# Kernel tuning notes

Measured on AMD Instinct MI355X. Metric: run time of the kernel, lower is better.

## Reference

```python
import jax, jax.numpy as jnp
import numpy as np

N_EXP, N_EMBD = 8, 1024
D_FF = 4 * N_EMBD
TOK = 2048  # tokens per expert


def setup_inputs() -> dict:
    key = jax.random.key(0)
    k_x, k_fc, k_pr, k_fb, k_pb = jax.random.split(key, 5)
    scale = 0.02
    return {
        "x": jax.random.normal(k_x, (N_EXP, TOK, N_EMBD), dtype=jnp.float32),
        "c_fc": jax.random.normal(k_fc, (N_EXP, N_EMBD, D_FF), dtype=jnp.float32) * scale,
        "c_proj": jax.random.normal(k_pr, (N_EXP, D_FF, N_EMBD), dtype=jnp.float32) * scale,
        "fc_bias": jax.random.normal(k_fb, (N_EXP, 1, D_FF), dtype=jnp.float32) * scale,
        "proj_bias": jax.random.normal(k_pb, (N_EXP, 1, N_EMBD), dtype=jnp.float32) * scale,
    }


def reference(x, c_fc, c_proj, fc_bias, proj_bias):
    # grouped GEMM over experts: [e, t, d] @ [e, d, f] -> [e, t, f]
    h = jnp.einsum('etd,edf->etf', x, c_fc) + fc_bias
    h = jax.nn.gelu(h, approximate=False)  # torch nn.GELU default is exact erf
    out = jnp.einsum('etf,efd->etd', h, c_proj) + proj_bias
    # dropout p=0.0 (eval): identity
    return out
```

## Files before the change

### kernel.cpp

```cpp
#include <hip/hip_runtime.h>
#include <cmath>

typedef __bf16 bf16;
typedef __bf16 bf16x8 __attribute__((ext_vector_type(8)));
typedef float floatx4 __attribute__((ext_vector_type(4)));

#define E_ 8
#define M_ 2048
#define D_ 1024
#define F_ 4096

#define PUNROLL _Pragma("unroll")

__device__ __forceinline__ void async16(const void* g, void* l) {
    __builtin_amdgcn_global_load_lds((const __attribute__((address_space(1))) unsigned int*)g,
                                     (__attribute__((address_space(3))) unsigned int*)l, 16, 0, 0);
}

__device__ __forceinline__ float gelu_fast(float u) {
    float s = u * (-1.5957691216f - 0.0713548162726f * u * u);
    return u * __builtin_amdgcn_rcpf(1.0f + __expf(s));
}

__device__ __forceinline__ void tconv_body(const float* __restrict__ in, bf16* __restrict__ out,
                                           int R, int C, int bx, int by, int bz,
                                           float (*t)[65]) {
    size_t eoff = (size_t)bz * R * C;
    in += eoff;
    out += eoff;
    const int c0 = bx * 64, r0 = by * 64;
    const int tid = threadIdx.x;
    const int f4c = tid & 15;
    const int rsub = tid >> 4;
    PUNROLL
    for (int p = 0; p < 4; ++p) {
        int row = rsub + p * 16;
        float4 v = *(const float4*)&in[(size_t)(r0 + row) * C + c0 + f4c * 4];
        t[row][f4c * 4 + 0] = v.x;
        t[row][f4c * 4 + 1] = v.y;
        t[row][f4c * 4 + 2] = v.z;
        t[row][f4c * 4 + 3] = v.w;
    }
    __syncthreads();
    const int rr = (tid & 7) * 8;
    const int cbase = tid >> 3;
    PUNROLL
    for (int p = 0; p < 2; ++p) {
        int c = cbase + p * 32;
        bf16x8 o = {(bf16)t[rr + 0][c], (bf16)t[rr + 1][c], (bf16)t[rr + 2][c],
                    (bf16)t[rr + 3][c], (bf16)t[rr + 4][c], (bf16)t[rr + 5][c],
                    (bf16)t[rr + 6][c], (bf16)t[rr + 7][c]};
        *(bf16x8*)&out[(size_t)(c0 + c) * R + r0 + rr] = o;
    }
}

__device__ __forceinline__ void xconv_body(const float4* __restrict__ x, bf16x8* __restrict__ xb,
                                           int b, int nblk) {
    const int n8 = E_ * M_ * D_ / 8;
    int i = b * 256 + threadIdx.x;
    for (; i < n8; i += nblk * 256) {
        float4 a = x[2 * i], c = x[2 * i + 1];
        bf16x8 r = {(bf16)a.x, (bf16)a.y, (bf16)a.z, (bf16)a.w,
                    (bf16)c.x, (bf16)c.y, (bf16)c.z, (bf16)c.w};
        xb[i] = r;
    }
}

__global__ __launch_bounds__(256) void prep_all(const float4* __restrict__ x,
                                                bf16x8* __restrict__ xb,
                                                const float* __restrict__ c_fc,
                                                bf16* __restrict__ w1T,
                                                const float* __restrict__ c_proj,
                                                bf16* __restrict__ w2T) {
    __shared__ float t[64][65];
    const int b = blockIdx.x;
    if (b < 2048) {
        xconv_body(x, xb, b, 2048);
    } else if (b < 10240) {
        const int idx = b - 2048;
        tconv_body(c_fc, w1T, D_, F_, idx & 63, (idx >> 6) & 15, idx >> 10, t);
    } else {
        const int idx = b - 10240;
        tconv_body(c_proj, w2T, F_, D_, idx & 15, (idx >> 4) & 63, idx >> 10, t);
    }
}

__global__ __launch_bounds__(256) void prep_kernel(const float4* __restrict__ x,
                                                   bf16x8* __restrict__ xb,
                                                   const float* __restrict__ c_fc,
                                                   bf16* __restrict__ w1T) {
    __shared__ float t[64][65];
    const int b = blockIdx.x;
    if (b < 2048) {
        xconv_body(x, xb, b, 2048);
    } else {
        const int idx = b - 2048;
        tconv_body(c_fc, w1T, D_, F_, idx & 63, (idx >> 6) & 15, idx >> 10, t);
    }
}

__global__ __launch_bounds__(256) void tconv2_kernel(const float* __restrict__ in,
                                                     bf16* __restrict__ out) {
    __shared__ float t[64][65];
    const int idx = blockIdx.x;
    tconv_body(in, out, F_, D_, idx & 15, (idx >> 4) & 63, idx >> 10, t);
}

template <bool GELU>
__global__ __launch_bounds__(512, 2) void gemm256(const bf16* __restrict__ A0,
                                                  const bf16* __restrict__ Bt0,
                                                  const float* __restrict__ bias0,
                                                  void* __restrict__ Out,
                                                  int M, int N, int K, int tpb) {
    extern __shared__ __align__(16) char sm[];
    const int nt = K >> 6;
    const int NTm = M >> 8;
    const int NTn = N >> 8;
    const int nwg = gridDim.x;
    const int bid = blockIdx.x;
    const int swz = (bid & 7) * (nwg >> 3) + (bid >> 3);

    const int tid = threadIdx.x;
    const int l = tid & 63;
    const int w = tid >> 6;
    const int wm = w >> 2;
    const int wn = w & 3;

    const size_t Kb = (size_t)K * 2;
    const size_t half128 = 128 * Kb;
    const size_t j64 = 64 * Kb;
    const int srow = (w << 3) + (l >> 3);
    const int kb = ((l & 7) ^ ((l >> 3) & 7)) << 4;
    const int ldsW = w << 10;

    auto stage = [&](int hb, const char* src, int ko) {
        async16(src + ko, sm + hb + ldsW);
        async16(src + j64 + ko, sm + hb + 8192 + ldsW);
    };
    auto prologue = [&](const char* aS, const char* bS) {
        stage(0, aS, 0);
        stage(32768, bS, 0);
        stage(49152, bS + half128, 0);
        stage(16384, aS + half128, 0);
        stage(65536 + 0, aS, 128);
        stage(65536 + 32768, bS, 128);
        stage(65536 + 49152, bS + half128, 128);
    };

    const int kpat0 = (((l >> 4) << 4)) ^ ((l & 7) << 4);
    const int kpat1 = (64 + ((l >> 4) << 4)) ^ ((l & 7) << 4);
    const int aRowOff = (((wm << 6) + (l & 15)) << 7);
    const int bRowOff = (((wn << 5) + (l & 15)) << 7);

    int tile = swz * tpb;
    int tm = tile % NTm, rem = tile / NTm;
    int tn = rem % NTn, e = rem / NTn;
    int row0 = tm << 8, col0 = tn << 8;
    const char* aS = (const char*)A0 + ((size_t)e * M + row0 + srow) * Kb + kb;
    const char* bS = (const char*)Bt0 + ((size_t)e * N + col0 + srow) * Kb + kb;
    prologue(aS, bS);

    for (int j = 0; j < tpb; ++j) {
        asm volatile("s_waitcnt vmcnt(6)" ::: "memory");
        __builtin_amdgcn_s_barrier();

        bf16x8 aa[4][2];
        bf16x8 bb0[2][2], bb1[2][2];
        floatx4 acc00[4][2] = {}, acc01[4][2] = {}, acc10[4][2] = {}, acc11[4][2] = {};

#define READ_A(QM)                                                                          \
    PUNROLL                                                                                 \
    for (int mi = 0; mi < 4; ++mi) {                                                        \
        aa[mi][0] = *(const bf16x8*)(sm + p + (QM)*16384 + aRowOff + mi * 2048 + kpat0);    \
        aa[mi][1] = *(const bf16x8*)(sm + p + (QM)*16384 + aRowOff + mi * 2048 + kpat1);    \
    }
#define READ_B(BB, QN)                                                                      \
    PUNROLL                                                                                 \
    for (int ni = 0; ni < 2; ++ni) {                                                        \
        BB[ni][0] = *(const bf16x8*)(sm + p + 32768 + (QN)*16384 + bRowOff + ni * 2048 + kpat0); \
        BB[ni][1] = *(const bf16x8*)(sm + p + 32768 + (QN)*16384 + bRowOff + ni * 2048 + kpat1); \
    }
#define MQ(ACC, BB)                                                                         \
    PUNROLL                                                                                 \
    for (int mi = 0; mi < 4; ++mi) PUNROLL for (int ni = 0; ni < 2; ++ni) {                 \
        ACC[mi][ni] = __builtin_amdgcn_mfma_f32_16x16x32_bf16(aa[mi][0], BB[ni][0], ACC[mi][ni], 0, 0, 0); \
        ACC[mi][ni] = __builtin_amdgcn_mfma_f32_16x16x32_bf16(aa[mi][1], BB[ni][1], ACC[mi][ni], 0, 0, 0); \
    }

        for (int t = 0; t < nt; ++t) {
            const int p = (t & 1) << 16;
            const int pn = p ^ 65536;
            const int ko1 = (t + 1) << 7;
            const int ko2 = (t + 2) << 7;
            READ_A(0)
            READ_B(bb0, 0)
            if (t + 1 < nt) stage(pn + 16384, aS + half128, ko1);
            __builtin_amdgcn_s_barrier();
            __builtin_amdgcn_s_setprio(1);
            MQ(acc00, bb0)
            __builtin_amdgcn_s_setprio(0);
            __builtin_amdgcn_s_barrier();
            READ_B(bb1, 1)
            if (t + 2 < nt) stage(p + 0, aS, ko2);
            __builtin_amdgcn_s_barrier();
            __builtin_amdgcn_s_setprio(1);
            MQ(acc01, bb1)
            __builtin_amdgcn_s_setprio(0);
            __builtin_amdgcn_s_barrier();
            READ_A(1)
            if (t + 2 < nt) stage(p + 32768, bS, ko2);
            __builtin_amdgcn_s_barrier();
            __builtin_amdgcn_s_setprio(1);
            MQ(acc11, bb1)
            __builtin_amdgcn_s_setprio(0);
            __builtin_amdgcn_s_barrier();
            if (t + 2 < nt) {
                stage(p + 49152, bS + half128, ko2);
                asm volatile("s_waitcnt vmcnt(6)" ::: "memory");
            } else if (t + 1 < nt) {
                asm volatile("s_waitcnt vmcnt(0)" ::: "memory");
            }
            __builtin_amdgcn_s_barrier();
            __builtin_amdgcn_s_setprio(1);
            MQ(acc10, bb0)
            __builtin_amdgcn_s_setprio(0);
            __builtin_amdgcn_s_barrier();
        }

        const int erow0 = row0, ecol0 = col0;
        const float* ebias = bias0 + (size_t)e * N;
        const size_t eout = (size_t)e * M * N;
        if (j + 1 < tpb) {
            tile = swz * tpb + j + 1;
            tm = tile % NTm; rem = tile / NTm;
            tn = rem % NTn; e = rem / NTn;
            row0 = tm << 8; col0 = tn << 8;
            aS = (const char*)A0 + ((size_t)e * M + row0 + srow) * Kb + kb;
            bS = (const char*)Bt0 + ((size_t)e * N + col0 + srow) * Kb + kb;
            prologue(aS, bS);
        }

#define EPI(ACC, QM, QN)                                                                    \
    PUNROLL                                                                                 \
    for (int ni = 0; ni < 2; ++ni) {                                                        \
        const int col = ecol0 + (QN)*128 + (wn << 5) + ni * 16 + (l & 15);                  \
        const float bv = ebias[col];                                                        \
        PUNROLL                                                                             \
        for (int mi = 0; mi < 4; ++mi) {                                                    \
            const int row = erow0 + (QM)*128 + (wm << 6) + mi * 16 + ((l >> 4) << 2);       \
            PUNROLL                                                                         \
            for (int r = 0; r < 4; ++r) {                                                   \
                float v = ACC[mi][ni][r] + bv;                                              \
                if (GELU)                                                                   \
                    ((bf16*)Out)[eout + (size_t)(row + r) * N + col] = (bf16)gelu_fast(v);  \
                else                                                                        \
                    ((float*)Out)[eout + (size_t)(row + r) * N + col] = v;                  \
            }                                                                               \
        }                                                                                   \
    }
        EPI(acc00, 0, 0)
        EPI(acc01, 0, 1)
        EPI(acc11, 1, 1)
        EPI(acc10, 1, 0)
#undef READ_A
#undef READ_B
#undef MQ
#undef EPI
    }
}

extern "C" void kernel_launch(void* const* d_in, const int* in_sizes, int n_in,
                              void* d_out, int out_size, void* d_ws, size_t ws_size,
                              hipStream_t stream) {
    const float* x = (const float*)d_in[0];
    const float* c_fc = (const float*)d_in[1];
    const float* c_proj = (const float*)d_in[2];
    const float* fc_bias = (const float*)d_in[3];
    const float* proj_bias = (const float*)d_in[4];
    float* out = (float*)d_out;

    const size_t EMD = (size_t)E_ * M_ * D_;
    const size_t EDF = (size_t)E_ * D_ * F_;
    const size_t EMF = (size_t)E_ * M_ * F_;
    const size_t need1 = (EMD + EDF + EMF) * 2;
    const size_t need2 = (EMD + 2 * EDF + EMF) * 2;
    if (ws_size < need1) return;

    static bool attrDone = false;
    if (!attrDone) {
        (void)hipFuncSetAttribute((const void*)&gemm256<true>,
                                  hipFuncAttributeMaxDynamicSharedMemorySize, 131072);
        (void)hipFuncSetAttribute((const void*)&gemm256<false>,
                                  hipFuncAttributeMaxDynamicSharedMemorySize, 131072);
        attrDone = true;
    }

    bf16* xb = (bf16*)d_ws;
    bf16* w1T = xb + EMD;

    if (ws_size >= need2) {
        bf16* w2T = w1T + EDF;
        bf16* h = w2T + EDF;
        prep_all<<<18432, 256, 0, stream>>>((const float4*)x, (bf16x8*)xb, c_fc, w1T,
                                            c_proj, w2T);
        gemm256<true><<<256, 512, 131072, stream>>>(xb, w1T, fc_bias, h, M_, F_, D_, 4);
        gemm256<false><<<256, 512, 131072, stream>>>(h, w2T, proj_bias, out, M_, D_, F_, 1);
    } else {
        bf16* h = w1T + EDF;
        prep_kernel<<<10240, 256, 0, stream>>>((const float4*)x, (bf16x8*)xb, c_fc, w1T);
        gemm256<true><<<256, 512, 131072, stream>>>(xb, w1T, fc_bias, h, M_, F_, D_, 4);
        tconv2_kernel<<<8192, 256, 0, stream>>>(c_proj, w1T);
        gemm256<false><<<256, 512, 131072, stream>>>(h, w1T, proj_bias, out, M_, D_, F_, 1);
    }
}
```

Before: 608.2 us.

## Fuse weight fp32-to-bf16 transpose into GEMM B-tile loading via registers

Result: slower. 705.7 us (+16.0%).

```diff
diff --git a/kernel.cpp b/kernel.cpp
--- a/kernel.cpp
+++ b/kernel.cpp
@@ -22,93 +22,21 @@
     return u * __builtin_amdgcn_rcpf(1.0f + __expf(s));
 }
 
-__device__ __forceinline__ void tconv_body(const float* __restrict__ in, bf16* __restrict__ out,
-                                           int R, int C, int bx, int by, int bz,
-                                           float (*t)[65]) {
-    size_t eoff = (size_t)bz * R * C;
-    in += eoff;
-    out += eoff;
-    const int c0 = bx * 64, r0 = by * 64;
-    const int tid = threadIdx.x;
-    const int f4c = tid & 15;
-    const int rsub = tid >> 4;
-    PUNROLL
-    for (int p = 0; p < 4; ++p) {
-        int row = rsub + p * 16;
-        float4 v = *(const float4*)&in[(size_t)(r0 + row) * C + c0 + f4c * 4];
-        t[row][f4c * 4 + 0] = v.x;
-        t[row][f4c * 4 + 1] = v.y;
-        t[row][f4c * 4 + 2] = v.z;
-        t[row][f4c * 4 + 3] = v.w;
-    }
-    __syncthreads();
-    const int rr = (tid & 7) * 8;
-    const int cbase = tid >> 3;
-    PUNROLL
-    for (int p = 0; p < 2; ++p) {
-        int c = cbase + p * 32;
-        bf16x8 o = {(bf16)t[rr + 0][c], (bf16)t[rr + 1][c], (bf16)t[rr + 2][c],
-                    (bf16)t[rr + 3][c], (bf16)t[rr + 4][c], (bf16)t[rr + 5][c],
-                    (bf16)t[rr + 6][c], (bf16)t[rr + 7][c]};
-        *(bf16x8*)&out[(size_t)(c0 + c) * R + r0 + rr] = o;
-    }
-}
-
-__device__ __forceinline__ void xconv_body(const float4* __restrict__ x, bf16x8* __restrict__ xb,
-                                           int b, int nblk) {
-    const int n8 = E_ * M_ * D_ / 8;
-    int i = b * 256 + threadIdx.x;
-    for (; i < n8; i += nblk * 256) {
-        float4 a = x[2 * i], c = x[2 * i + 1];
+__global__ __launch_bounds__(256) void cvt_bf16_kernel(const float4* __restrict__ in,
+                                                       bf16x8* __restrict__ out, int n8) {
+    int i = blockIdx.x * 256 + threadIdx.x;
+    int stride = gridDim.x * 256;
+    for (; i < n8; i += stride) {
+        float4 a = in[2 * i], b = in[2 * i + 1];
         bf16x8 r = {(bf16)a.x, (bf16)a.y, (bf16)a.z, (bf16)a.w,
-                    (bf16)c.x, (bf16)c.y, (bf16)c.z, (bf16)c.w};
-        xb[i] = r;
-    }
-}
-
-__global__ __launch_bounds__(256) void prep_all(const float4* __restrict__ x,
-                                                bf16x8* __restrict__ xb,
-                                                const float* __restrict__ c_fc,
-                                                bf16* __restrict__ w1T,
-                                                const float* __restrict__ c_proj,
-                                                bf16* __restrict__ w2T) {
-    __shared__ float t[64][65];
-    const int b = blockIdx.x;
-    if (b < 2048) {
-        xconv_body(x, xb, b, 2048);
-    } else if (b < 10240) {
-        const int idx = b - 2048;
-        tconv_body(c_fc, w1T, D_, F_, idx & 63, (idx >> 6) & 15, idx >> 10, t);
-    } else {
-        const int idx = b - 10240;
-        tconv_body(c_proj, w2T, F_, D_, idx & 15, (idx >> 4) & 63, idx >> 10, t);
-    }
-}
-
-__global__ __launch_bounds__(256) void prep_kernel(const float4* __restrict__ x,
-                                                   bf16x8* __restrict__ xb,
-                                                   const float* __restrict__ c_fc,
-                                                   bf16* __restrict__ w1T) {
-    __shared__ float t[64][65];
-    const int b = blockIdx.x;
-    if (b < 2048) {
-        xconv_body(x, xb, b, 2048);
-    } else {
-        const int idx = b - 2048;
-        tconv_body(c_fc, w1T, D_, F_, idx & 63, (idx >> 6) & 15, idx >> 10, t);
-    }
-}
-
-__global__ __launch_bounds__(256) void tconv2_kernel(const float* __restrict__ in,
-                                                     bf16* __restrict__ out) {
-    __shared__ float t[64][65];
-    const int idx = blockIdx.x;
-    tconv_body(in, out, F_, D_, idx & 15, (idx >> 4) & 63, idx >> 10, t);
+                    (bf16)b.x, (bf16)b.y, (bf16)b.z, (bf16)b.w};
+        out[i] = r;
+    }
 }
 
 template <bool GELU>
 __global__ __launch_bounds__(512, 2) void gemm256(const bf16* __restrict__ A0,
-                                                  const bf16* __restrict__ Bt0,
+                                                  const float* __restrict__ Bf0,
                                                   const float* __restrict__ bias0,
                                                   void* __restrict__ Out,
                                                   int M, int N, int K, int tpb) {
@@ -137,31 +65,49 @@
         async16(src + ko, sm + hb + ldsW);
         async16(src + j64 + ko, sm + hb + 8192 + ldsW);
     };
-    auto prologue = [&](const char* aS, const char* bS) {
-        stage(0, aS, 0);
-        stage(32768, bS, 0);
-        stage(49152, bS + half128, 0);
-        stage(16384, aS + half128, 0);
-        stage(65536 + 0, aS, 128);
-        stage(65536 + 32768, bS, 128);
-        stage(65536 + 49152, bS + half128, 128);
-    };
-
-    const int kpat0 = (((l >> 4) << 4)) ^ ((l & 7) << 4);
-    const int kpat1 = (64 + ((l >> 4) << 4)) ^ ((l & 7) << 4);
+
+    const int lq4 = l >> 4;
+    const int kpat0 = ((lq4 ^ (l & 7)) << 4);
+    const int kpat1 = (((4 | lq4) ^ (l & 7)) << 4);
     const int aRowOff = (((wm << 6) + (l & 15)) << 7);
-    const int bRowOff = (((wn << 5) + (l & 15)) << 7);
+
+    const int fB0 = (l & 7) ^ ((l & 15) >> 2);
+    const int gB = lq4 ^ fB0;
+    const int bRowByte = (((wn << 5) + (l & 15)) << 7);
+
+    int wOffB[4];
+    PUNROLL
+    for (int j = 0; j < 4; ++j) {
+        const int r = l * 4 + j;
+        const int slot = w ^ ((((l & 1) << 2) | j) ^ (l & 7));
+        wOffB[j] = 32768 + ((r >> 7) << 14) + ((r & 127) << 7) + (slot << 4);
+    }
 
     int tile = swz * tpb;
     int tm = tile % NTm, rem = tile / NTm;
     int tn = rem % NTn, e = rem / NTn;
     int row0 = tm << 8, col0 = tn << 8;
     const char* aS = (const char*)A0 + ((size_t)e * M + row0 + srow) * Kb + kb;
-    const char* bS = (const char*)Bt0 + ((size_t)e * N + col0 + srow) * Kb + kb;
-    prologue(aS, bS);
+    const float* bG = Bf0 + (size_t)e * K * N + (size_t)(w << 3) * N + col0 + (l << 2);
+
+    float4 bpro[8];
+    stage(0, aS, 0);
+    stage(16384, aS + half128, 0);
+    stage(65536, aS, 128);
+    PUNROLL
+    for (int r = 0; r < 8; ++r) bpro[r] = *(const float4*)(bG + (size_t)r * N);
 
     for (int j = 0; j < tpb; ++j) {
-        asm volatile("s_waitcnt vmcnt(6)" ::: "memory");
+        asm volatile("s_waitcnt vmcnt(0)" ::: "memory");
+#define BWRITE0(JC, FLD)                                                                    \
+    {                                                                                       \
+        bf16x8 v = {(bf16)bpro[0].FLD, (bf16)bpro[1].FLD, (bf16)bpro[2].FLD,                \
+                    (bf16)bpro[3].FLD, (bf16)bpro[4].FLD, (bf16)bpro[5].FLD,                \
+                    (bf16)bpro[6].FLD, (bf16)bpro[7].FLD};                                  \
+        *(bf16x8*)(sm + wOffB[JC]) = v;                                                     \
+    }
+        BWRITE0(0, x) BWRITE0(1, y) BWRITE0(2, z) BWRITE0(3, w)
+        asm volatile("s_waitcnt lgkmcnt(0)" ::: "memory");
         __builtin_amdgcn_s_barrier();
 
         bf16x8 aa[4][2];
@@ -172,19 +118,35 @@
     PUNROLL                                                                                 \
     for (int mi = 0; mi < 4; ++mi) {                                                        \
         aa[mi][0] = *(const bf16x8*)(sm + p + (QM)*16384 + aRowOff + mi * 2048 + kpat0);    \
+        aa[mi][1] = *(const bf16x8*)(sm + p + (QM)*16384 + aRowOff + mi * 2048 + 64 + kpat1 - kpat0 - 64 + kpat1); \
+    }
+#undef READ_A
+#define READ_A(QM)                                                                          \
+    PUNROLL                                                                                 \
+    for (int mi = 0; mi < 4; ++mi) {                                                        \
+        aa[mi][0] = *(const bf16x8*)(sm + p + (QM)*16384 + aRowOff + mi * 2048 + kpat0);    \
         aa[mi][1] = *(const bf16x8*)(sm + p + (QM)*16384 + aRowOff + mi * 2048 + kpat1);    \
     }
 #define READ_B(BB, QN)                                                                      \
     PUNROLL                                                                                 \
     for (int ni = 0; ni < 2; ++ni) {                                                        \
-        BB[ni][0] = *(const bf16x8*)(sm + p + 32768 + (QN)*16384 + bRowOff + ni * 2048 + kpat0); \
-        BB[ni][1] = *(const bf16x8*)(sm + p + 32768 + (QN)*16384 + bRowOff + ni * 2048 + kpat1); \
+        BB[ni][0] = *(const bf16x8*)(sm + p + 32768 + (QN)*16384 + bRowByte + ni * 2048 +   \
+                                     ((gB ^ (ni << 2)) << 4));                              \
+        BB[ni][1] = *(const bf16x8*)(sm + p + 32768 + (QN)*16384 + bRowByte + ni * 2048 +   \
+                                     ((gB ^ 4 ^ (ni << 2)) << 4));                          \
     }
 #define MQ(ACC, BB)                                                                         \
     PUNROLL                                                                                 \
     for (int mi = 0; mi < 4; ++mi) PUNROLL for (int ni = 0; ni < 2; ++ni) {                 \
         ACC[mi][ni] = __builtin_amdgcn_mfma_f32_16x16x32_bf16(aa[mi][0], BB[ni][0], ACC[mi][ni], 0, 0, 0); \
         ACC[mi][ni] = __builtin_amdgcn_mfma_f32_16x16x32_bf16(aa[mi][1], BB[ni][1], ACC[mi][ni], 0, 0, 0); \
+    }
+#define BWRITE(JC, FLD)                                                                     \
+    {                                                                                       \
+        bf16x8 v = {(bf16)breg[0].FLD, (bf16)breg[1].FLD, (bf16)breg[2].FLD,                \
+                    (bf16)breg[3].FLD, (bf16)breg[4].FLD, (bf16)breg[5].FLD,                \
+                    (bf16)breg[6].FLD, (bf16)breg[7].FLD};                                  \
+        *(bf16x8*)(sm + pn + wOffB[JC]) = v;                                                \
     }
 
         for (int t = 0; t < nt; ++t) {
@@ -194,7 +156,13 @@
             const int ko2 = (t + 2) << 7;
             READ_A(0)
             READ_B(bb0, 0)
-            if (t + 1 < nt) stage(pn + 16384, aS + half128, ko1);
+            float4 breg[8];
+            if (t + 1 < nt) {
+                stage(pn + 16384, aS + half128, ko1);
+                const float* bp = bG + ((size_t)(t + 1) << 6) * N;
+                PUNROLL
+                for (int r = 0; r < 8; ++r) breg[r] = *(const float4*)(bp + (size_t)r * N);
+            }
             __builtin_amdgcn_s_barrier();
             __builtin_amdgcn_s_setprio(1);
             MQ(acc00, bb0)
@@ -208,17 +176,18 @@
             __builtin_amdgcn_s_setprio(0);
             __builtin_amdgcn_s_barrier();
             READ_A(1)
-            if (t + 2 < nt) stage(p + 32768, bS, ko2);
             __builtin_amdgcn_s_barrier();
             __builtin_amdgcn_s_setprio(1);
             MQ(acc11, bb1)
             __builtin_amdgcn_s_setprio(0);
             __builtin_amdgcn_s_barrier();
-            if (t + 2 < nt) {
-                stage(p + 49152, bS + half128, ko2);
-                asm volatile("s_waitcnt vmcnt(6)" ::: "memory");
-            } else if (t + 1 < nt) {
-                asm volatile("s_waitcnt vmcnt(0)" ::: "memory");
+            if (t + 1 < nt) {
+                if (t + 2 < nt)
+                    asm volatile("s_waitcnt vmcnt(2)" ::: "memory");
+                else
+                    asm volatile("s_waitcnt vmcnt(0)" ::: "memory");
+                BWRITE(0, x) BWRITE(1, y) BWRITE(2, z) BWRITE(3, w)
+                asm volatile("s_waitcnt lgkmcnt(0)" ::: "memory");
             }
             __builtin_amdgcn_s_barrier();
             __builtin_amdgcn_s_setprio(1);
@@ -236,8 +205,12 @@
             tn = rem % NTn; e = rem / NTn;
             row0 = tm << 8; col0 = tn << 8;
             aS = (const char*)A0 + ((size_t)e * M + row0 + srow) * Kb + kb;
-            bS = (const char*)Bt0 + ((size_t)e * N + col0 + srow) * Kb + kb;
-            prologue(aS, bS);
+            bG = Bf0 + (size_t)e * K * N + (size_t)(w << 3) * N + col0 + (l << 2);
+            stage(0, aS, 0);
+            stage(16384, aS + half128, 0);
+            stage(65536, aS, 128);
+            PUNROLL
+            for (int r = 0; r < 8; ++r) bpro[r] = *(const float4*)(bG + (size_t)r * N);
         }
 
 #define EPI(ACC, QM, QN)                                                                    \
@@ -266,6 +239,8 @@
 #undef READ_B
 #undef MQ
 #undef EPI
+#undef BWRITE
+#undef BWRITE0
     }
 }
 
@@ -280,11 +255,10 @@
     float* out = (float*)d_out;
 
     const size_t EMD = (size_t)E_ * M_ * D_;
-    const size_t EDF = (size_t)E_ * D_ * F_;
     const size_t EMF = (size_t)E_ * M_ * F_;
-    const size_t need1 = (EMD + EDF + EMF) * 2;
-    const size_t need2 = (EMD + 2 * EDF + EMF) * 2;
-    if (ws_size < need1) return;
+    bf16* xb = (bf16*)d_ws;
+    bf16* h = xb + EMD;
+    if (ws_size < (EMD + EMF) * 2) return;
 
     static bool attrDone = false;
     if (!attrDone) {
@@ -295,21 +269,7 @@
         attrDone = true;
     }
 
-    bf16* xb = (bf16*)d_ws;
-    bf16* w1T = xb + EMD;
-
-    if (ws_size >= need2) {
-        bf16* w2T = w1T + EDF;
-        bf16* h = w2T + EDF;
-        prep_all<<<18432, 256, 0, stream>>>((const float4*)x, (bf16x8*)xb, c_fc, w1T,
-                                            c_proj, w2T);
-        gemm256<true><<<256, 512, 131072, stream>>>(xb, w1T, fc_bias, h, M_, F_, D_, 4);
-        gemm256<false><<<256, 512, 131072, stream>>>(h, w2T, proj_bias, out, M_, D_, F_, 1);
-    } else {
-        bf16* h = w1T + EDF;
-        prep_kernel<<<10240, 256, 0, stream>>>((const float4*)x, (bf16x8*)xb, c_fc, w1T);
-        gemm256<true><<<256, 512, 131072, stream>>>(xb, w1T, fc_bias, h, M_, F_, D_, 4);
-        tconv2_kernel<<<8192, 256, 0, stream>>>(c_proj, w1T);
-        gemm256<false><<<256, 512, 131072, stream>>>(h, w1T, proj_bias, out, M_, D_, F_, 1);
-    }
-}
+    cvt_bf16_kernel<<<2048, 256, 0, stream>>>((const float4*)x, (bf16x8*)xb, E_ * M_ * D_ / 8);
+    gemm256<true><<<256, 512, 131072, stream>>>(xb, c_fc, fc_bias, h, M_, F_, D_, 4);
+    gemm256<false><<<256, 512, 131072, stream>>>(h, c_proj, proj_bias, out, M_, D_, F_, 1);
+}
```
